# Optimization experiments

Measured on AMD Instinct MI355X. Metric: run time of the kernel, lower is better.

## Reference

```python
import jax, jax.numpy as jnp
import numpy as np

B, S_IMG, S_TXT = 1, 3072, 512
D_MODEL, H, D_HEAD = 3072, 24, 128
INNER = H * D_HEAD
EPS = 1e-5


def rms_norm(x, w):
    # x: [..., D_HEAD]
    var = jnp.mean(jnp.square(x), axis=-1, keepdims=True)
    return x * jax.lax.rsqrt(var + EPS) * w


def apply_rope(x, cos, sin):
    # x: [B,S,H,D]; cos/sin: [S,D]; interleaved (non-neox) rotation
    x1 = x[..., 0::2]
    x2 = x[..., 1::2]
    rot = jnp.stack([-x2, x1], axis=-1).reshape(x.shape)
    c = cos[None, :, None, :]
    s = sin[None, :, None, :]
    return x * c + rot * s


def setup_inputs() -> dict:
    key = jax.random.key(0)
    ks = jax.random.split(key, 12)
    sc = 1.0 / np.sqrt(D_MODEL)
    ang = jax.random.uniform(ks[10], (S_TXT + S_IMG, D_HEAD), jnp.float32, 0.0, 2 * np.pi)
    return {
        "hidden_states": jax.random.normal(ks[0], (B, S_IMG, D_MODEL), jnp.float32),
        "encoder_hidden_states": jax.random.normal(ks[1], (B, S_TXT, D_MODEL), jnp.float32),
        "cos": jnp.cos(ang),
        "sin": jnp.sin(ang),
        "W_qkv": jax.random.normal(ks[2], (3 * INNER, D_MODEL), jnp.float32) * sc,
        "W_add_qkv": jax.random.normal(ks[3], (3 * INNER, D_MODEL), jnp.float32) * sc,
        "b_add_qkv": jnp.zeros((3 * INNER,), jnp.float32),
        "norm_q_w": jnp.ones((D_HEAD,), jnp.float32),
        "norm_k_w": jnp.ones((D_HEAD,), jnp.float32),
        "norm_add_q_w": jnp.ones((D_HEAD,), jnp.float32),
        "norm_add_k_w": jnp.ones((D_HEAD,), jnp.float32),
        "W_out": jax.random.normal(ks[4], (D_MODEL, INNER), jnp.float32) * sc,
        "b_out": jnp.zeros((D_MODEL,), jnp.float32),
        "W_add_out": jax.random.normal(ks[5], (D_MODEL, INNER), jnp.float32) * sc,
        "b_add_out": jnp.zeros((D_MODEL,), jnp.float32),
    }


def reference(hidden_states, encoder_hidden_states, cos, sin,
              W_qkv, W_add_qkv, b_add_qkv,
              norm_q_w, norm_k_w, norm_add_q_w, norm_add_k_w,
              W_out, b_out, W_add_out, b_add_out):
    # fused QKV projections
    qkv = jnp.einsum('bsd,ed->bse', hidden_states, W_qkv)
    q, k, v = jnp.split(qkv, 3, axis=-1)
    eqkv = jnp.einsum('bsd,ed->bse', encoder_hidden_states, W_add_qkv) + b_add_qkv
    eq, ek, ev = jnp.split(eqkv, 3, axis=-1)

    def heads(x):
        return x.reshape(x.shape[0], x.shape[1], H, D_HEAD)

    q, k, v = heads(q), heads(k), heads(v)
    eq, ek, ev = heads(eq), heads(ek), heads(ev)

    # per-head RMSNorm on queries/keys
    q = rms_norm(q, norm_q_w)
    k = rms_norm(k, norm_k_w)
    eq = rms_norm(eq, norm_add_q_w)
    ek = rms_norm(ek, norm_add_k_w)

    # joint concat: text first, then image
    q = jnp.concatenate([eq, q], axis=1)
    k = jnp.concatenate([ek, k], axis=1)
    v = jnp.concatenate([ev, v], axis=1)

    # RoPE on full joint sequence
    q = apply_rope(q, cos, sin)
    k = apply_rope(k, cos, sin)

    # non-causal softmax attention, scale = 1/sqrt(head_dim)
    scale = 1.0 / np.sqrt(D_HEAD)
    scores = jnp.einsum('bqhd,bkhd->bhqk', q, k) * scale
    probs = jax.nn.softmax(scores, axis=-1)
    out = jnp.einsum('bhqk,bkhd->bqhd', probs, v)  # [B,S,H,D]
    out = out.reshape(out.shape[0], out.shape[1], INNER)

    enc_out = out[:, :S_TXT]
    img_out = out[:, S_TXT:]
    enc_out = jnp.einsum('bse,de->bsd', enc_out, W_add_out) + b_add_out
    img_out = jnp.einsum('bse,de->bsd', img_out, W_out) + b_out
    return (img_out, enc_out)
```

## Files before the change

kernel.cpp:

```cpp
#include <hip/hip_runtime.h>


typedef unsigned short u16;
typedef __attribute__((ext_vector_type(2))) unsigned short u16x2;
typedef __attribute__((ext_vector_type(4))) unsigned short u16x4;
typedef __attribute__((ext_vector_type(8))) unsigned short u16x8;
typedef __attribute__((ext_vector_type(8))) short bf16x8;
typedef __attribute__((ext_vector_type(4))) float f32x4;

#define DEV __device__ __forceinline__

DEV u16 f2bf(float f) {
  unsigned u = __builtin_bit_cast(unsigned, f);
  u = (u + 0x7FFFu + ((u >> 16) & 1u)) >> 16;
  return (u16)u;
}
DEV float bf2f(u16 s) { return __builtin_bit_cast(float, (unsigned)s << 16); }

DEV void store_out(u16* p, float v)  { *p = f2bf(v); }
DEV void store_out(float* p, float v) { *p = v; }

#define AS1(p) (const __attribute__((address_space(1))) void*)(p)
#define AS3(p) (__attribute__((address_space(3))) void*)(p)
#define GLL16(g, l) __builtin_amdgcn_global_load_lds(AS1(g), AS3(l), 16, 0, 0)

#define BAR() do { asm volatile("" ::: "memory"); __builtin_amdgcn_s_barrier(); \
                   asm volatile("" ::: "memory"); } while (0)
#define VMC8() asm volatile("s_waitcnt vmcnt(8)" ::: "memory")
#define VMC4() asm volatile("s_waitcnt vmcnt(4)" ::: "memory")
#define VMC0() asm volatile("s_waitcnt vmcnt(0)" ::: "memory")

__global__ __launch_bounds__(256) void cvt_kernel(const float* __restrict__ src,
                                                  u16* __restrict__ dst, int n4) {
  int i = blockIdx.x * blockDim.x + threadIdx.x;
  int stride = gridDim.x * blockDim.x;
  for (; i < n4; i += stride) {
    float4 v = reinterpret_cast<const float4*>(src)[i];
    u16x4 o;
    o.x = f2bf(v.x); o.y = f2bf(v.y); o.z = f2bf(v.z); o.w = f2bf(v.w);
    reinterpret_cast<u16x4*>(dst)[i] = o;
  }
}

template <typename OT>
__global__ __launch_bounds__(512, 2) void gemm256(
    const u16* __restrict__ A,
    const u16* __restrict__ Bimg, const u16* __restrict__ Benc,
    const float* __restrict__ biasImg, const float* __restrict__ biasEnc,
    OT* __restrict__ Cimg, OT* __restrict__ Cenc,
    int N, int K, int split, int nwg) {
  const int bid = blockIdx.x;
  const int swz = (bid & 7) * (nwg >> 3) + (bid >> 3);
  const int ntn = N >> 8;
  const int mt = swz / ntn, nt = swz % ntn;
  const int m0 = mt << 8, n0 = nt << 8;
  const u16* B = (m0 < split) ? Benc : Bimg;
  const float* bias = (m0 < split) ? biasEnc : biasImg;

  __shared__ u16 lds[2][2][16384];

  const int tid = threadIdx.x, w = tid >> 6, lane = tid & 63;
  const int wm = w >> 2, wn = w & 3;
  const int q = lane & 15, hi = lane >> 4;
  const size_t ldb = (size_t)K * 2;

  f32x4 acc[8][4];
#pragma unroll
  for (int i = 0; i < 8; ++i)
#pragma unroll
    for (int j = 0; j < 4; ++j)
#pragma unroll
      for (int r = 0; r < 4; ++r) acc[i][j][r] = 0.f;

  auto STAGE = [&](int d, int kt) {
    const char* sA = (const char*)A + (size_t)m0 * ldb + kt * 128;
    const char* sB = (const char*)B + (size_t)n0 * ldb + kt * 128;
    char* dA = (char*)&lds[d][0][0];
    char* dB = (char*)&lds[d][1][0];
#pragma unroll
    for (int j = 0; j < 4; ++j) {
      int base = j * 8192 + w * 1024;
      int off = base + lane * 16;
      int row = off >> 7;
      int src = (off & 127) ^ ((row & 7) << 4);
      GLL16(sA + (size_t)row * ldb + src, dA + base);
      GLL16(sB + (size_t)row * ldb + src, dB + base);
    }
  };
  auto LDA = [&](int d, int i, int ks) -> bf16x8 {
    int row = wm * 128 + i * 16 + q;
    int cb = ks * 64 + hi * 16;
    return *(const bf16x8*)((const char*)&lds[d][0][0] + row * 128 + (cb ^ ((row & 7) << 4)));
  };
  auto LDB = [&](int d, int j, int ks) -> bf16x8 {
    int row = wn * 64 + j * 16 + q;
    int cb = ks * 64 + hi * 16;
    return *(const bf16x8*)((const char*)&lds[d][1][0] + row * 128 + (cb ^ ((row & 7) << 4)));
  };

  auto HALF = [&](int d) {
    bf16x8 bfr[4][2];
#pragma unroll
    for (int ph = 0; ph < 4; ++ph) {
      if (ph == 0) {
#pragma unroll
        for (int j = 0; j < 4; ++j)
#pragma unroll
          for (int ks = 0; ks < 2; ++ks) bfr[j][ks] = LDB(d, j, ks);
      }
      bf16x8 af[2][2];
#pragma unroll
      for (int m = 0; m < 2; ++m)
#pragma unroll
        for (int ks = 0; ks < 2; ++ks) af[m][ks] = LDA(d, 2 * ph + m, ks);
      __builtin_amdgcn_s_setprio(1);
#pragma unroll
      for (int m = 0; m < 2; ++m)
#pragma unroll
        for (int j = 0; j < 4; ++j)
#pragma unroll
          for (int ks = 0; ks < 2; ++ks)
            acc[2 * ph + m][j] = __builtin_amdgcn_mfma_f32_16x16x32_bf16(
                af[m][ks], bfr[j][ks], acc[2 * ph + m][j], 0, 0, 0);
      __builtin_amdgcn_s_setprio(0);
      if (ph < 3) BAR();
    }
  };

  const int NT2 = K >> 7;
  STAGE(0, 0);
  STAGE(1, 1);
  VMC8();
  BAR();
  for (int t = 0; t < NT2; ++t) {
    HALF(0);
    BAR();
    if (t + 1 < NT2) { STAGE(0, 2 * t + 2); VMC8(); }
    else             VMC0();
    BAR();
    HALF(1);
    BAR();
    if (t + 1 < NT2) { STAGE(1, 2 * t + 3); VMC8(); }
    else             VMC0();
    BAR();
  }

#pragma unroll
  for (int i = 0; i < 8; ++i) {
    int rbase = m0 + wm * 128 + i * 16 + (hi << 2);
#pragma unroll
    for (int j = 0; j < 4; ++j) {
      int col = n0 + wn * 64 + j * 16 + q;
      float bv = bias ? bias[col] : 0.f;
#pragma unroll
      for (int r = 0; r < 4; ++r) {
        int row = rbase + r;
        float v = acc[i][j][r] + bv;
        if (row < split) store_out(&Cenc[(size_t)row * N + col], v);
        else             store_out(&Cimg[(size_t)(row - split) * N + col], v);
      }
    }
  }
}

__global__ __launch_bounds__(256) void norm_rope(
    u16* __restrict__ qkv, u16* __restrict__ vt,
    const float* __restrict__ cosT, const float* __restrict__ sinT,
    const float* __restrict__ nqw_img, const float* __restrict__ nkw_img,
    const float* __restrict__ nqw_enc, const float* __restrict__ nkw_enc) {
  const int h = blockIdx.y;
  const int s0 = blockIdx.x * 64;
  const int tid = threadIdx.x, w = tid >> 6, lane = tid & 63;
  const bool enc = (s0 < 512);
  const float* nqw = enc ? nqw_enc : nqw_img;
  const float* nkw = enc ? nkw_enc : nkw_img;
  const float SCL = 0.12751743f;
  const float wq0 = nqw[2 * lane], wq1 = nqw[2 * lane + 1];
  const float wk0 = nkw[2 * lane], wk1 = nkw[2 * lane + 1];
  u16x8 va0, va1, vb0, vb1;
#pragma unroll
  for (int r = 0; r < 16; ++r) {
    const int s = s0 + w * 16 + r;
    const size_t rowb = (size_t)s * 9216 + h * 128 + 2 * lane;
    float2 cv = *(const float2*)&cosT[(size_t)s * 128 + 2 * lane];
    float2 sv = *(const float2*)&sinT[(size_t)s * 128 + 2 * lane];
    {
      u16x2 qu = *(u16x2*)&qkv[rowb];
      float x0 = bf2f(qu.x), x1 = bf2f(qu.y);
      float ss = x0 * x0 + x1 * x1;
#pragma unroll
      for (int d = 1; d < 64; d <<= 1) ss += __shfl_xor(ss, d);
      float rms = rsqrtf(ss * (1.0f / 128.0f) + 1e-5f);
      x0 *= rms * wq0; x1 *= rms * wq1;
      float o0 = (x0 * cv.x - x1 * sv.x) * SCL;
      float o1 = (x1 * cv.y + x0 * sv.y) * SCL;
      u16x2 ou; ou.x = f2bf(o0); ou.y = f2bf(o1);
      *(u16x2*)&qkv[rowb] = ou;
    }
    {
      u16x2 ku = *(u16x2*)&qkv[rowb + 3072];
      float x0 = bf2f(ku.x), x1 = bf2f(ku.y);
      float ss = x0 * x0 + x1 * x1;
#pragma unroll
      for (int d = 1; d < 64; d <<= 1) ss += __shfl_xor(ss, d);
      float rms = rsqrtf(ss * (1.0f / 128.0f) + 1e-5f);
      x0 *= rms * wk0; x1 *= rms * wk1;
      float o0 = x0 * cv.x - x1 * sv.x;
      float o1 = x1 * cv.y + x0 * sv.y;
      u16x2 ou; ou.x = f2bf(o0); ou.y = f2bf(o1);
      *(u16x2*)&qkv[rowb + 3072] = ou;
    }
    {
      u16x2 vu = *(u16x2*)&qkv[rowb + 6144];
      if (r < 8) { va0[r] = vu.x; vb0[r] = vu.y; }
      else       { va1[r - 8] = vu.x; vb1[r - 8] = vu.y; }
    }
  }
  const size_t vbase = (size_t)h * 128 * 3584 + (size_t)(2 * lane) * 3584 + s0 + w * 16;
  *(u16x8*)&vt[vbase]            = va0;
  *(u16x8*)&vt[vbase + 8]        = va1;
  *(u16x8*)&vt[vbase + 3584]     = vb0;
  *(u16x8*)&vt[vbase + 3584 + 8] = vb1;
}

__global__ __launch_bounds__(256, 4) void attn_kernel(
    const u16* __restrict__ qkv, const u16* __restrict__ vt,
    u16* __restrict__ aout) {
  const int bid = blockIdx.x;
  const int qt = bid / 24;
  const int rr = bid % 24;
  const int h = (rr % 8) * 3 + (rr / 8);
  const int tid = threadIdx.x, w = tid >> 6, lane = tid & 63;
  const int qbase = qt * 64 + w * 16;
  const int q = lane & 15, hi = lane >> 4;
  __shared__ u16 Klds[8192];
  __shared__ u16 Vlds[8192];
  __shared__ u16 Plds[4][1024];

  bf16x8 aq[4];
  {
    const u16* qp = qkv + (size_t)(qbase + q) * 9216 + h * 128 + (hi << 3);
#pragma unroll
    for (int ks = 0; ks < 4; ++ks) aq[ks] = *(const bf16x8*)(qp + ks * 32);
  }
  float m_i = -1e30f, l_i = 0.f;
  f32x4 o[8];
#pragma unroll
  for (int dt = 0; dt < 8; ++dt)
#pragma unroll
    for (int r = 0; r < 4; ++r) o[dt][r] = 0.f;
  const size_t vhead = (size_t)h * 128 * 3584;

  auto STAGE_K = [&](int kt0) {
    const char* src = (const char*)(qkv + (size_t)(kt0 + w * 16 + q) * 9216 + 3072 + h * 128) + (hi << 4);
    char* dst = (char*)Klds + w * 4096 + lane * 16;
#pragma unroll
    for (int j = 0; j < 4; ++j) GLL16(src + j * 64, dst + j * 1024);
  };
  auto STAGE_V = [&](int kt0) {
    const char* vsrc = (const char*)(vt + vhead + kt0) + (hi << 4);
    char* dst = (char*)Vlds + w * 4096 + lane * 16;
#pragma unroll
    for (int j = 0; j < 4; ++j)
      GLL16(vsrc + (size_t)((w * 2 + (j >> 1)) * 16 + q) * 7168 + (j & 1) * 64, dst + j * 1024);
  };

  const int NT = 56;
  STAGE_K(0);
  STAGE_V(0);
  VMC4();
  BAR();
  for (int t = 0; t < NT; ++t) {
    f32x4 sacc[4];
#pragma unroll
    for (int kt = 0; kt < 4; ++kt)
#pragma unroll
      for (int r = 0; r < 4; ++r) sacc[kt][r] = 0.f;
    __builtin_amdgcn_s_setprio(1);
#pragma unroll
    for (int kt = 0; kt < 4; ++kt) {
      bf16x8 bk[4];
#pragma unroll
      for (int ks = 0; ks < 4; ++ks)
        bk[ks] = *(const bf16x8*)((const char*)Klds + kt * 4096 + ks * 1024 + hi * 256 + q * 16);
#pragma unroll
      for (int ks = 0; ks < 4; ++ks)
        sacc[kt] = __builtin_amdgcn_mfma_f32_16x16x32_bf16(bk[ks], aq[ks], sacc[kt], 0, 0, 0);
    }
    __builtin_amdgcn_s_setprio(0);
    BAR();
    if (t + 1 < NT) { STAGE_K((t + 1) * 64); VMC4(); }
    else            VMC0();
    BAR();

    float mx = sacc[0][0];
#pragma unroll
    for (int kt = 0; kt < 4; ++kt)
#pragma unroll
      for (int r = 0; r < 4; ++r) mx = fmaxf(mx, sacc[kt][r]);
    mx = fmaxf(mx, __shfl_xor(mx, 16));
    mx = fmaxf(mx, __shfl_xor(mx, 32));
    if (!__all(mx - m_i <= 8.f)) {
      float mnew = fmaxf(m_i, mx);
      float alpha = __builtin_amdgcn_exp2f(m_i - mnew);
      m_i = mnew;
      l_i *= alpha;
#pragma unroll
      for (int r = 0; r < 4; ++r) {
        float ar = __shfl(alpha, (lane & 48) | ((hi << 2) + r));
#pragma unroll
        for (int dt = 0; dt < 8; ++dt) o[dt][r] *= ar;
      }
    }
    float psum = 0.f;
#pragma unroll
    for (int kt = 0; kt < 4; ++kt) {
      u16x4 pw;
#pragma unroll
      for (int r = 0; r < 4; ++r) {
        float p = __builtin_amdgcn_exp2f(sacc[kt][r] - m_i);
        psum += p;
        pw[r] = (u16)(__builtin_bit_cast(unsigned, p) >> 16);
      }
      const int c = kt * 2 + (hi >> 1);
      *(u16x4*)((char*)Plds[w] + ((c >> 2) * 1024 + (c & 3) * 256 + q * 16 + (hi & 1) * 8)) = pw;
    }
    psum += __shfl_xor(psum, 16);
    psum += __shfl_xor(psum, 32);
    l_i += psum;

    bf16x8 pa[2];
#pragma unroll
    for (int ks = 0; ks < 2; ++ks)
      pa[ks] = *(const bf16x8*)((const char*)Plds[w] + ks * 1024 + hi * 256 + q * 16);
    __builtin_amdgcn_s_setprio(1);
#pragma unroll
    for (int dt = 0; dt < 8; ++dt) {
      bf16x8 bv[2];
#pragma unroll
      for (int ks = 0; ks < 2; ++ks)
        bv[ks] = *(const bf16x8*)((const char*)Vlds + dt * 2048 + ks * 1024 + hi * 256 + q * 16);
      o[dt] = __builtin_amdgcn_mfma_f32_16x16x32_bf16(pa[0], bv[0], o[dt], 0, 0, 0);
      o[dt] = __builtin_amdgcn_mfma_f32_16x16x32_bf16(pa[1], bv[1], o[dt], 0, 0, 0);
    }
    __builtin_amdgcn_s_setprio(0);
    BAR();
    if (t + 1 < NT) { STAGE_V((t + 1) * 64); VMC4(); }
    else            VMC0();
    BAR();
  }

#pragma unroll
  for (int r = 0; r < 4; ++r) {
    const int q2 = (hi << 2) + r;
    const float lr = __shfl(l_i, (lane & 48) | q2);
    const float inv = 1.0f / lr;
    const int s = qbase + q2;
#pragma unroll
    for (int dt = 0; dt < 8; ++dt) {
      aout[(size_t)s * 3072 + h * 128 + dt * 16 + q] = f2bf(o[dt][r] * inv);
    }
  }
}

extern "C" void kernel_launch(void* const* d_in, const int* in_sizes, int n_in,
                              void* d_out, int out_size, void* d_ws, size_t ws_size,
                              hipStream_t stream) {
  (void)in_sizes; (void)n_in; (void)out_size; (void)ws_size;
  const float* hs    = (const float*)d_in[0];
  const float* ehs   = (const float*)d_in[1];
  const float* cosT  = (const float*)d_in[2];
  const float* sinT  = (const float*)d_in[3];
  const float* Wqkv  = (const float*)d_in[4];
  const float* Wadd  = (const float*)d_in[5];
  const float* bAdd  = (const float*)d_in[6];
  const float* nqw   = (const float*)d_in[7];
  const float* nkw   = (const float*)d_in[8];
  const float* naqw  = (const float*)d_in[9];
  const float* nakw  = (const float*)d_in[10];
  const float* Wout  = (const float*)d_in[11];
  const float* bout  = (const float*)d_in[12];
  const float* Waddo = (const float*)d_in[13];
  const float* baddo = (const float*)d_in[14];

  char* ws = (char*)d_ws;
  u16* Ain = (u16*)(ws);
  u16* WqI = (u16*)(ws + 22020096);
  u16* WqE = WqI + (size_t)9216 * 3072;
  u16* WoI = (u16*)(ws + 135266304);
  u16* WoE = WoI + (size_t)3072 * 3072;
  u16* qkv = (u16*)(ws + 173015040);
  u16* vt   = Ain;
  u16* aout = WqI;

  cvt_kernel<<<1024, 256, 0, stream>>>(ehs,   Ain,                      512 * 3072 / 4);
  cvt_kernel<<<1024, 256, 0, stream>>>(hs,    Ain + (size_t)512 * 3072, 3072 * 3072 / 4);
  cvt_kernel<<<2048, 256, 0, stream>>>(Wqkv,  WqI, 9216 * 3072 / 4);
  cvt_kernel<<<2048, 256, 0, stream>>>(Wadd,  WqE, 9216 * 3072 / 4);
  cvt_kernel<<<1024, 256, 0, stream>>>(Wout,  WoI, 3072 * 3072 / 4);
  cvt_kernel<<<1024, 256, 0, stream>>>(Waddo, WoE, 3072 * 3072 / 4);

  gemm256<u16><<<dim3(504), 512, 0, stream>>>(Ain, WqI, WqE, nullptr, bAdd,
                                              qkv + (size_t)512 * 9216, qkv, 9216, 3072, 512, 504);
  norm_rope<<<dim3(56, 24), 256, 0, stream>>>(qkv, vt, cosT, sinT, nqw, nkw, naqw, nakw);
  attn_kernel<<<dim3(1344), 256, 0, stream>>>(qkv, vt, aout);
  float* outp = (float*)d_out;
  gemm256<float><<<dim3(168), 512, 0, stream>>>(aout, WoI, WoE, bout, baddo,
                                                outp, outp + (size_t)3072 * 3072, 3072, 3072, 512, 168);
}
```

Baseline: 757.4 us.

## Rework attention to 32x32 MFMA tiles with register P and double-buffered K/V

The attention kernel moves from 16x16x32 to 32x32x16 bf16 MFMAs, with 32 queries per wave and 128 per block, which halves the grid. Probabilities are packed to bf16 in registers using cvt_pk and permlane32_swap, so the LDS round trip for P goes away. K and V tiles are double-buffered and the next tiles are prefetched two steps ahead, which drops two barriers per iteration. The costs are more registers (occupancy hint lowered to 2), fewer blocks to fill the CUs, and P is now rounded to bf16 instead of truncated.

```diff
diff --git a/kernel.cpp b/kernel.cpp
--- a/kernel.cpp
+++ b/kernel.cpp
@@ -7,6 +7,8 @@
 typedef __attribute__((ext_vector_type(8))) unsigned short u16x8;
 typedef __attribute__((ext_vector_type(8))) short bf16x8;
 typedef __attribute__((ext_vector_type(4))) float f32x4;
+typedef __attribute__((ext_vector_type(16))) float f32x16;
+typedef __attribute__((ext_vector_type(4))) unsigned u32x4;
 
 #define DEV __device__ __forceinline__
 
@@ -27,7 +29,6 @@
 #define BAR() do { asm volatile("" ::: "memory"); __builtin_amdgcn_s_barrier(); \
                    asm volatile("" ::: "memory"); } while (0)
 #define VMC8() asm volatile("s_waitcnt vmcnt(8)" ::: "memory")
-#define VMC4() asm volatile("s_waitcnt vmcnt(4)" ::: "memory")
 #define VMC0() asm volatile("s_waitcnt vmcnt(0)" ::: "memory")
 
 __global__ __launch_bounds__(256) void cvt_kernel(const float* __restrict__ src,
@@ -223,7 +224,7 @@
   *(u16x8*)&vt[vbase + 3584 + 8] = vb1;
 }
 
-__global__ __launch_bounds__(256, 4) void attn_kernel(
+__global__ __launch_bounds__(256, 2) void attn_kernel(
     const u16* __restrict__ qkv, const u16* __restrict__ vt,
     u16* __restrict__ aout) {
   const int bid = blockIdx.x;
@@ -231,74 +232,84 @@
   const int rr = bid % 24;
   const int h = (rr % 8) * 3 + (rr / 8);
   const int tid = threadIdx.x, w = tid >> 6, lane = tid & 63;
-  const int qbase = qt * 64 + w * 16;
-  const int q = lane & 15, hi = lane >> 4;
-  __shared__ u16 Klds[8192];
-  __shared__ u16 Vlds[8192];
-  __shared__ u16 Plds[4][1024];
-
-  bf16x8 aq[4];
+  const int q32 = lane & 31, hi5 = lane >> 5;
+  const int qbase = qt * 128 + w * 32;
+  __shared__ u16 Klds[2][8192];
+  __shared__ u16 Vlds[2][8192];
+
+  bf16x8 aq[8];
   {
-    const u16* qp = qkv + (size_t)(qbase + q) * 9216 + h * 128 + (hi << 3);
-#pragma unroll
-    for (int ks = 0; ks < 4; ++ks) aq[ks] = *(const bf16x8*)(qp + ks * 32);
+    const u16* qp = qkv + (size_t)(qbase + q32) * 9216 + h * 128 + hi5 * 8;
+#pragma unroll
+    for (int ds = 0; ds < 8; ++ds) aq[ds] = *(const bf16x8*)(qp + ds * 16);
   }
   float m_i = -1e30f, l_i = 0.f;
-  f32x4 o[8];
-#pragma unroll
-  for (int dt = 0; dt < 8; ++dt)
-#pragma unroll
-    for (int r = 0; r < 4; ++r) o[dt][r] = 0.f;
+  f32x16 o[4];
+#pragma unroll
+  for (int dt = 0; dt < 4; ++dt)
+#pragma unroll
+    for (int r = 0; r < 16; ++r) o[dt][r] = 0.f;
   const size_t vhead = (size_t)h * 128 * 3584;
 
-  auto STAGE_K = [&](int kt0) {
-    const char* src = (const char*)(qkv + (size_t)(kt0 + w * 16 + q) * 9216 + 3072 + h * 128) + (hi << 4);
-    char* dst = (char*)Klds + w * 4096 + lane * 16;
-#pragma unroll
-    for (int j = 0; j < 4; ++j) GLL16(src + j * 64, dst + j * 1024);
-  };
-  auto STAGE_V = [&](int kt0) {
-    const char* vsrc = (const char*)(vt + vhead + kt0) + (hi << 4);
-    char* dst = (char*)Vlds + w * 4096 + lane * 16;
+  auto STAGE_K = [&](int kt0, int b) {
+    const int kt = w >> 1;
+    const char* src = (const char*)(qkv + (size_t)(kt0 + kt * 32 + q32) * 9216 + 3072 + h * 128) + hi5 * 16;
+    char* dst = (char*)Klds[b] + kt * 8192 + (w & 1) * 4096 + lane * 16;
 #pragma unroll
     for (int j = 0; j < 4; ++j)
-      GLL16(vsrc + (size_t)((w * 2 + (j >> 1)) * 16 + q) * 7168 + (j & 1) * 64, dst + j * 1024);
+      GLL16(src + ((w & 1) * 4 + j) * 32, dst + j * 1024);
+  };
+  auto STAGE_V = [&](int kt0, int b) {
+    const char* src = (const char*)(vt + vhead + (size_t)(w * 32 + q32) * 3584 + kt0) + hi5 * 16;
+    char* dst = (char*)Vlds[b] + w * 4096 + lane * 16;
+#pragma unroll
+    for (int j = 0; j < 4; ++j)
+      GLL16(src + j * 32, dst + j * 1024);
+  };
+
+  auto PACK = [&](const float* p, bf16x8* out2) {
+    unsigned w0[4], w1[4];
+#pragma unroll
+    for (int g = 0; g < 4; ++g) {
+      asm("v_cvt_pk_bf16_f32 %0, %1, %2" : "=v"(w0[g]) : "v"(p[4 * g + 0]), "v"(p[4 * g + 1]));
+      asm("v_cvt_pk_bf16_f32 %0, %1, %2" : "=v"(w1[g]) : "v"(p[4 * g + 2]), "v"(p[4 * g + 3]));
+    }
+    asm("v_permlane32_swap_b32 %0, %1" : "+v"(w0[0]), "+v"(w0[1]));
+    asm("v_permlane32_swap_b32 %0, %1" : "+v"(w1[0]), "+v"(w1[1]));
+    asm("v_permlane32_swap_b32 %0, %1" : "+v"(w0[2]), "+v"(w0[3]));
+    asm("v_permlane32_swap_b32 %0, %1" : "+v"(w1[2]), "+v"(w1[3]));
+    u32x4 lo = {w0[0], w1[0], w0[1], w1[1]};
+    u32x4 hi_ = {w0[2], w1[2], w0[3], w1[3]};
+    out2[0] = __builtin_bit_cast(bf16x8, lo);
+    out2[1] = __builtin_bit_cast(bf16x8, hi_);
   };
 
   const int NT = 56;
-  STAGE_K(0);
-  STAGE_V(0);
-  VMC4();
-  BAR();
+  STAGE_K(0, 0);   STAGE_V(0, 0);
+  STAGE_K(64, 1);  STAGE_V(64, 1);
   for (int t = 0; t < NT; ++t) {
-    f32x4 sacc[4];
-#pragma unroll
-    for (int kt = 0; kt < 4; ++kt)
-#pragma unroll
-      for (int r = 0; r < 4; ++r) sacc[kt][r] = 0.f;
+    const int b = t & 1;
+    if (t + 1 < NT) VMC8(); else VMC0();
+    BAR();
+
+    f32x16 s0, s1;
+#pragma unroll
+    for (int r = 0; r < 16; ++r) { s0[r] = 0.f; s1[r] = 0.f; }
     __builtin_amdgcn_s_setprio(1);
 #pragma unroll
-    for (int kt = 0; kt < 4; ++kt) {
-      bf16x8 bk[4];
-#pragma unroll
-      for (int ks = 0; ks < 4; ++ks)
-        bk[ks] = *(const bf16x8*)((const char*)Klds + kt * 4096 + ks * 1024 + hi * 256 + q * 16);
-#pragma unroll
-      for (int ks = 0; ks < 4; ++ks)
-        sacc[kt] = __builtin_amdgcn_mfma_f32_16x16x32_bf16(bk[ks], aq[ks], sacc[kt], 0, 0, 0);
+    for (int ds = 0; ds < 8; ++ds) {
+      bf16x8 k0 = *(const bf16x8*)((const char*)Klds[b] + ds * 1024 + lane * 16);
+      bf16x8 k1 = *(const bf16x8*)((const char*)Klds[b] + 8192 + ds * 1024 + lane * 16);
+      s0 = __builtin_amdgcn_mfma_f32_32x32x16_bf16(k0, aq[ds], s0, 0, 0, 0);
+      s1 = __builtin_amdgcn_mfma_f32_32x32x16_bf16(k1, aq[ds], s1, 0, 0, 0);
     }
     __builtin_amdgcn_s_setprio(0);
-    BAR();
-    if (t + 1 < NT) { STAGE_K((t + 1) * 64); VMC4(); }
-    else            VMC0();
-    BAR();
-
-    float mx = sacc[0][0];
-#pragma unroll
-    for (int kt = 0; kt < 4; ++kt)
-#pragma unroll
-      for (int r = 0; r < 4; ++r) mx = fmaxf(mx, sacc[kt][r]);
-    mx = fmaxf(mx, __shfl_xor(mx, 16));
+
+    float mx = s0[0];
+#pragma unroll
+    for (int r = 1; r < 16; ++r) mx = fmaxf(mx, s0[r]);
+#pragma unroll
+    for (int r = 0; r < 16; ++r) mx = fmaxf(mx, s1[r]);
     mx = fmaxf(mx, __shfl_xor(mx, 32));
     if (!__all(mx - m_i <= 8.f)) {
       float mnew = fmaxf(m_i, mx);
@@ -306,60 +317,49 @@
       m_i = mnew;
       l_i *= alpha;
 #pragma unroll
-      for (int r = 0; r < 4; ++r) {
-        float ar = __shfl(alpha, (lane & 48) | ((hi << 2) + r));
-#pragma unroll
-        for (int dt = 0; dt < 8; ++dt) o[dt][r] *= ar;
+      for (int r = 0; r < 16; ++r) {
+        int qr = (r & 3) + 8 * (r >> 2) + 4 * hi5;
+        float ar = __shfl(alpha, qr);
+#pragma unroll
+        for (int dt = 0; dt < 4; ++dt) o[dt][r] *= ar;
       }
     }
+    float p0[16], p1[16];
     float psum = 0.f;
 #pragma unroll
-    for (int kt = 0; kt < 4; ++kt) {
-      u16x4 pw;
-#pragma unroll
-      for (int r = 0; r < 4; ++r) {
-        float p = __builtin_amdgcn_exp2f(sacc[kt][r] - m_i);
-        psum += p;
-        pw[r] = (u16)(__builtin_bit_cast(unsigned, p) >> 16);
-      }
-      const int c = kt * 2 + (hi >> 1);
-      *(u16x4*)((char*)Plds[w] + ((c >> 2) * 1024 + (c & 3) * 256 + q * 16 + (hi & 1) * 8)) = pw;
-    }
-    psum += __shfl_xor(psum, 16);
+    for (int r = 0; r < 16; ++r) { p0[r] = __builtin_amdgcn_exp2f(s0[r] - m_i); psum += p0[r]; }
+#pragma unroll
+    for (int r = 0; r < 16; ++r) { p1[r] = __builtin_amdgcn_exp2f(s1[r] - m_i); psum += p1[r]; }
     psum += __shfl_xor(psum, 32);
     l_i += psum;
 
-    bf16x8 pa[2];
-#pragma unroll
-    for (int ks = 0; ks < 2; ++ks)
-      pa[ks] = *(const bf16x8*)((const char*)Plds[w] + ks * 1024 + hi * 256 + q * 16);
+    bf16x8 pa[4];
+    PACK(p0, &pa[0]);
+    PACK(p1, &pa[2]);
+
     __builtin_amdgcn_s_setprio(1);
 #pragma unroll
-    for (int dt = 0; dt < 8; ++dt) {
-      bf16x8 bv[2];
-#pragma unroll
-      for (int ks = 0; ks < 2; ++ks)
-        bv[ks] = *(const bf16x8*)((const char*)Vlds + dt * 2048 + ks * 1024 + hi * 256 + q * 16);
-      o[dt] = __builtin_amdgcn_mfma_f32_16x16x32_bf16(pa[0], bv[0], o[dt], 0, 0, 0);
-      o[dt] = __builtin_amdgcn_mfma_f32_16x16x32_bf16(pa[1], bv[1], o[dt], 0, 0, 0);
+    for (int dt = 0; dt < 4; ++dt) {
+#pragma unroll
+      for (int ks = 0; ks < 4; ++ks) {
+        bf16x8 bv = *(const bf16x8*)((const char*)Vlds[b] + dt * 4096 + ks * 1024 + lane * 16);
+        o[dt] = __builtin_amdgcn_mfma_f32_32x32x16_bf16(pa[ks], bv, o[dt], 0, 0, 0);
+      }
     }
     __builtin_amdgcn_s_setprio(0);
     BAR();
-    if (t + 1 < NT) { STAGE_V((t + 1) * 64); VMC4(); }
-    else            VMC0();
-    BAR();
-  }
-
-#pragma unroll
-  for (int r = 0; r < 4; ++r) {
-    const int q2 = (hi << 2) + r;
-    const float lr = __shfl(l_i, (lane & 48) | q2);
+    if (t + 2 < NT) { STAGE_K((t + 2) * 64, b); STAGE_V((t + 2) * 64, b); }
+  }
+
+#pragma unroll
+  for (int r = 0; r < 16; ++r) {
+    const int qr = (r & 3) + 8 * (r >> 2) + 4 * hi5;
+    const float lr = __shfl(l_i, qr);
     const float inv = 1.0f / lr;
-    const int s = qbase + q2;
-#pragma unroll
-    for (int dt = 0; dt < 8; ++dt) {
-      aout[(size_t)s * 3072 + h * 128 + dt * 16 + q] = f2bf(o[dt][r] * inv);
-    }
+    const size_t srow = (size_t)(qbase + qr) * 3072 + h * 128 + q32;
+#pragma unroll
+    for (int dt = 0; dt < 4; ++dt)
+      aout[srow + dt * 32] = f2bf(o[dt][r] * inv);
   }
 }
 
@@ -403,7 +403,7 @@
   gemm256<u16><<<dim3(504), 512, 0, stream>>>(Ain, WqI, WqE, nullptr, bAdd,
                                               qkv + (size_t)512 * 9216, qkv, 9216, 3072, 512, 504);
   norm_rope<<<dim3(56, 24), 256, 0, stream>>>(qkv, vt, cosT, sinT, nqw, nkw, naqw, nakw);
-  attn_kernel<<<dim3(1344), 256, 0, stream>>>(qkv, vt, aout);
+  attn_kernel<<<dim3(672), 256, 0, stream>>>(qkv, vt, aout);
   float* outp = (float*)d_out;
   gemm256<float><<<dim3(168), 512, 0, stream>>>(aout, WoI, WoE, bout, baddo,
                                                 outp, outp + (size_t)3072 * 3072, 3072, 3072, 512, 168);
```

After: 705.7 us. 1.07x faster.
